# Performance work log

Measured on AMD Instinct MI355X. Metric: run time of the kernel, lower is better.

The kernel has to match this reference:

```python
import jax, jax.numpy as jnp
from jax import lax
import numpy as np

NEG = -1e30  # safe log-space -inf for fp32 (avoids inf-inf NaNs)
EPS = 1e-7   # keras.backend.epsilon()


def setup_inputs() -> dict:
    key = jax.random.key(0)
    k1, k2 = jax.random.split(key)
    B, T, C, L = 512, 512, 96, 64
    y_true = jax.random.randint(k1, (B, L), 0, C - 1, dtype=jnp.int64)  # labels in [0, C-2]
    # y_pred mimics softmax output: positive, rows sum to 1
    logits = jax.random.uniform(k2, (B, T, C), dtype=jnp.float32)
    y_pred = logits / jnp.sum(logits, axis=-1, keepdims=True)
    return {"y_true": y_true, "y_pred": y_pred}


def _ctc_batch_cost(y_true, y_pred):
    # Faithful to keras.backend.ctc_batch_cost with full input/label lengths
    # and blank index = num_classes - 1.
    B, T, C = y_pred.shape
    L = y_true.shape[1]
    blank = C - 1
    S = 2 * L + 1  # extended label length: blanks interleaved

    logp = jnp.log(y_pred + EPS)  # [B, T, C]

    # extended label sequence: blank, l0, blank, l1, ..., blank
    ext = jnp.full((B, S), blank, dtype=y_true.dtype).at[:, 1::2].set(y_true)  # [B, S]

    # log-probs of extended labels at every time step: [T, B, S]
    lp = jnp.take_along_axis(
        logp, jnp.broadcast_to(ext[:, None, :], (B, T, S)), axis=2
    ).transpose(1, 0, 2)

    # skip transition (s-2 -> s) allowed iff ext[s] != blank and ext[s] != ext[s-2]
    skip = jnp.concatenate(
        [jnp.zeros((B, 2), dtype=bool),
         (ext[:, 2:] != blank) & (ext[:, 2:] != ext[:, :-2])],
        axis=1,
    )  # [B, S]

    # init: alpha_0(0) = logp(blank), alpha_0(1) = logp(l0)
    alpha0 = jnp.full((B, S), NEG, dtype=logp.dtype)
    alpha0 = alpha0.at[:, 0].set(lp[0, :, 0]).at[:, 1].set(lp[0, :, 1])

    def step(alpha, lp_t):
        s1 = jnp.pad(alpha[:, :-1], ((0, 0), (1, 0)), constant_values=NEG)
        s2 = jnp.pad(alpha[:, :-2], ((0, 0), (2, 0)), constant_values=NEG)
        a = jnp.logaddexp(alpha, s1)
        a = jnp.where(skip, jnp.logaddexp(a, s2), a)
        return a + lp_t, None

    alpha, _ = lax.scan(step, alpha0, lp[1:])
    loss = -jnp.logaddexp(alpha[:, -1], alpha[:, -2])  # [B]
    return loss[:, None]  # [B, 1], matching ctc_batch_cost


def reference(y_true, y_pred):
    return _ctc_batch_cost(y_true, y_pred)
```

## Files before the change

kernel.cpp:

```cpp
#include <hip/hip_runtime.h>
#include <math.h>


constexpr int Bv = 512;
constexpr int Tv = 512;
constexpr int Cv = 96;
constexpr int Lv = 64;
constexpr int BLANK = Cv - 1;
constexpr float EPSf = 1e-7f;

constexpr int ROWS = 32;
constexpr int NCH  = Tv / ROWS;
constexpr int CF   = ROWS * Cv;
constexpr int RS   = 100;
constexpr int LBUF = ROWS * RS;

__device__ __forceinline__ float dpp_shr1(float x) {
    return __int_as_float(
        __builtin_amdgcn_update_dpp(0, __float_as_int(x), 0x138, 0xf, 0xf, true));
}
template <int C>
__device__ __forceinline__ float dppmax(float m) {
    return fmaxf(m, __int_as_float(
        __builtin_amdgcn_update_dpp(0, __float_as_int(m), C, 0xf, 0xf, true)));
}

__global__ void __launch_bounds__(64, 1) ctc_fwd(const int* __restrict__ y_true,
                                                 const float* __restrict__ y_pred,
                                                 float* __restrict__ out) {
    __shared__ float lds[2 * LBUF];

    const int b = blockIdx.x;
    const int l = threadIdx.x;
    const float* __restrict__ yp = y_pred + (size_t)b * (Tv * Cv);

    const int lab   = y_true[b * Lv + l];
    const int labm1 = __shfl_up(lab, 1);
    const bool skip = (l > 0) && (lab != labm1);

#define WA(i) ((((i)*64 + l) / 24) * 400 + (((i)*64 + l) % 24) * 16)
    const int wa0 = WA(0),  wa1 = WA(1),  wa2 = WA(2),  wa3 = WA(3);
    const int wa4 = WA(4),  wa5 = WA(5),  wa6 = WA(6),  wa7 = WA(7);
    const int wa8 = WA(8),  wa9 = WA(9), wa10 = WA(10), wa11 = WA(11);
#undef WA

    float4 G0, G1, G2, G3, G4, G5, G6, G7, G8, G9, G10, G11;
    float4 H0, H1, H2, H3, H4, H5, H6, H7, H8, H9, H10, H11;
#define GLOADS(S, g) do { const float* gp_ = (g) + l * 4;                    \
    S##0 = *(const float4*)(gp_ +    0); S##1 = *(const float4*)(gp_ +  256);\
    S##2 = *(const float4*)(gp_ +  512); S##3 = *(const float4*)(gp_ +  768);\
    S##4 = *(const float4*)(gp_ + 1024); S##5 = *(const float4*)(gp_ + 1280);\
    S##6 = *(const float4*)(gp_ + 1536); S##7 = *(const float4*)(gp_ + 1792);\
    S##8 = *(const float4*)(gp_ + 2048); S##9 = *(const float4*)(gp_ + 2304);\
    S##10= *(const float4*)(gp_ + 2560); S##11= *(const float4*)(gp_ + 2816);} while (0)
#define E4(v) make_float4((v).x + EPSf, (v).y + EPSf, (v).z + EPSf, (v).w + EPSf)
#define SWRITES(S, bufn) do { char* p_ = (char*)(bufn);                      \
    *(float4*)(p_ + wa0) = E4(S##0);  *(float4*)(p_ + wa1) = E4(S##1);       \
    *(float4*)(p_ + wa2) = E4(S##2);  *(float4*)(p_ + wa3) = E4(S##3);       \
    *(float4*)(p_ + wa4) = E4(S##4);  *(float4*)(p_ + wa5) = E4(S##5);       \
    *(float4*)(p_ + wa6) = E4(S##6);  *(float4*)(p_ + wa7) = E4(S##7);       \
    *(float4*)(p_ + wa8) = E4(S##8);  *(float4*)(p_ + wa9) = E4(S##9);       \
    *(float4*)(p_ + wa10)= E4(S##10); *(float4*)(p_ + wa11)= E4(S##11); } while (0)

    float AB0,AB1,AB2,AB3,AB4,AB5,AB6,AB7, AL0,AL1,AL2,AL3,AL4,AL5,AL6,AL7;
    float BB0,BB1,BB2,BB3,BB4,BB5,BB6,BB7, BL0,BL1,BL2,BL3,BL4,BL5,BL6,BL7;
#define LOAD8(P, bb, r0) do { const float* pB_ = (bb) + BLANK;               \
    const float* pL_ = (bb) + lab;                                           \
    P##B0 = pB_[((r0)+0)*RS]; P##L0 = pL_[((r0)+0)*RS];                      \
    P##B1 = pB_[((r0)+1)*RS]; P##L1 = pL_[((r0)+1)*RS];                      \
    P##B2 = pB_[((r0)+2)*RS]; P##L2 = pL_[((r0)+2)*RS];                      \
    P##B3 = pB_[((r0)+3)*RS]; P##L3 = pL_[((r0)+3)*RS];                      \
    P##B4 = pB_[((r0)+4)*RS]; P##L4 = pL_[((r0)+4)*RS];                      \
    P##B5 = pB_[((r0)+5)*RS]; P##L5 = pL_[((r0)+5)*RS];                      \
    P##B6 = pB_[((r0)+6)*RS]; P##L6 = pL_[((r0)+6)*RS];                      \
    P##B7 = pB_[((r0)+7)*RS]; P##L7 = pL_[((r0)+7)*RS]; } while (0)

    float a0, a1, a2;
    int   e_acc = 0;
    float sc_p = 1.0f; int e_p = 0;

    auto step = [&](float pb, float pl) {
        float pls = skip ? pl : 0.0f;
        float a1p = dpp_shr1(a1);
        float t01 = a0 + a1;
        float na1 = fmaf(a1p, pls, t01 * pl);
        float na0 = fmaf(a1p, pb, a0 * pb);
        float na2 = (a2 + a1) * pb;
        a0 = na0; a1 = na1; a2 = na2;
    };
    auto rn_apply = [&]() {
        a0 *= sc_p; a1 *= sc_p; a2 *= sc_p; e_acc += e_p;
    };
    auto rn_compute = [&]() {
        float m = fmaxf(fmaxf(a0, a1), a2);
        m = dppmax<0x111>(m); m = dppmax<0x112>(m); m = dppmax<0x114>(m);
        m = dppmax<0x118>(m); m = dppmax<0x142>(m); m = dppmax<0x143>(m);
        float mw = __int_as_float(__builtin_amdgcn_readlane(__float_as_int(m), 63));
        int e; (void)frexpf(mw, &e);
        sc_p = ldexpf(1.0f, -e); e_p = e;
    };
#define GROUP8(P) do {                                                       \
    step(P##B0, P##L0); step(P##B1, P##L1); step(P##B2, P##L2);              \
    step(P##B3, P##L3); rn_apply();                                          \
    step(P##B4, P##L4); step(P##B5, P##L5); step(P##B6, P##L6);              \
    step(P##B7, P##L7); rn_compute(); } while (0)

    GLOADS(G, yp);
    GLOADS(H, yp + CF);
    SWRITES(G, lds);
    GLOADS(G, yp + 2 * CF);
    LOAD8(A, lds, 0);
    const bool lane0 = (l == 0);
    a0 = lane0 ? AB0 : 0.0f;
    a1 = lane0 ? AL0 : 0.0f;
    a2 = 0.0f;

    float* const buf0 = lds;
    float* const buf1 = lds + LBUF;

    for (int c = 0; c < NCH; c += 2) {
        LOAD8(B, buf0, 8);
        if (c == 0) {
            step(AB1, AL1); step(AB2, AL2); step(AB3, AL3); rn_apply();
            step(AB4, AL4); step(AB5, AL5); step(AB6, AL6); step(AB7, AL7);
            rn_compute();
        } else {
            GROUP8(A);
        }
        LOAD8(A, buf0, 16);
        GROUP8(B);
        LOAD8(B, buf0, 24);
        GROUP8(A);
        SWRITES(H, buf1);
        if (c + 3 < NCH) GLOADS(H, yp + (size_t)(c + 3) * CF);
        LOAD8(A, buf1, 0);
        GROUP8(B);

        LOAD8(B, buf1, 8);
        GROUP8(A);
        LOAD8(A, buf1, 16);
        GROUP8(B);
        LOAD8(B, buf1, 24);
        GROUP8(A);
        if (c + 1 < NCH - 1) SWRITES(G, buf0);
        if (c + 4 < NCH) GLOADS(G, yp + (size_t)(c + 4) * CF);
        if (c + 1 < NCH - 1) LOAD8(A, buf0, 0);
        GROUP8(B);
    }

    if (l == 63) {
        float sum = a1 + a2;
        out[b] = -(logf(sum) + (float)e_acc * 0.69314718055994530942f);
    }
#undef GLOADS
#undef SWRITES
#undef E4
#undef LOAD8
#undef GROUP8
}

extern "C" void kernel_launch(void* const* d_in, const int* in_sizes, int n_in,
                              void* d_out, int out_size, void* d_ws, size_t ws_size,
                              hipStream_t stream) {
    const int*   y_true = (const int*)d_in[0];
    const float* y_pred = (const float*)d_in[1];
    float*       out    = (float*)d_out;
    (void)in_sizes; (void)n_in; (void)out_size; (void)d_ws; (void)ws_size;
    ctc_fwd<<<Bv, 64, 0, stream>>>(y_true, y_pred, out);
}
```

Measured before the change: 149.8 us.

## Split producer and consumer into separate wavefronts with double-buffered LDS

The block grows to two wavefronts. One wave only streams y_pred chunks from global memory into the LDS double buffer, and the other runs the CTC alpha recursion from LDS, with __syncthreads between halves. The goal is to take global-load issue and LDS writes off the latency-critical recursion wave so the two overlap on separate waves. In exchange, each half-chunk now costs a block barrier, and the grid uses more waves per CU.

```diff
diff --git a/kernel.cpp b/kernel.cpp
--- a/kernel.cpp
+++ b/kernel.cpp
@@ -25,13 +25,15 @@
         __builtin_amdgcn_update_dpp(0, __float_as_int(m), C, 0xf, 0xf, true)));
 }
 
-__global__ void __launch_bounds__(64, 1) ctc_fwd(const int* __restrict__ y_true,
-                                                 const float* __restrict__ y_pred,
-                                                 float* __restrict__ out) {
+__global__ void __launch_bounds__(128, 1) ctc_fwd(const int* __restrict__ y_true,
+                                                  const float* __restrict__ y_pred,
+                                                  float* __restrict__ out) {
     __shared__ float lds[2 * LBUF];
 
-    const int b = blockIdx.x;
-    const int l = threadIdx.x;
+    const int b   = blockIdx.x;
+    const int tid = threadIdx.x;
+    const int wid = tid >> 6;
+    const int l   = tid & 63;
     const float* __restrict__ yp = y_pred + (size_t)b * (Tv * Cv);
 
     const int lab   = y_true[b * Lv + l];
@@ -78,6 +80,7 @@
     float a0, a1, a2;
     int   e_acc = 0;
     float sc_p = 1.0f; int e_p = 0;
+    const bool lane0 = (l == 0);
 
     auto step = [&](float pb, float pl) {
         float pls = skip ? pl : 0.0f;
@@ -105,50 +108,55 @@
     step(P##B4, P##L4); step(P##B5, P##L5); step(P##B6, P##L6);              \
     step(P##B7, P##L7); rn_compute(); } while (0)
 
-    GLOADS(G, yp);
-    GLOADS(H, yp + CF);
-    SWRITES(G, lds);
-    GLOADS(G, yp + 2 * CF);
-    LOAD8(A, lds, 0);
-    const bool lane0 = (l == 0);
-    a0 = lane0 ? AB0 : 0.0f;
-    a1 = lane0 ? AL0 : 0.0f;
-    a2 = 0.0f;
+#define CONSUME(bb, FIRST) do {                                              \
+    LOAD8(A, (bb), 0);                                                       \
+    LOAD8(B, (bb), 8);                                                       \
+    if (FIRST) {                                                             \
+        a0 = lane0 ? AB0 : 0.0f;          \
+        a1 = lane0 ? AL0 : 0.0f;                                             \
+        a2 = 0.0f;                                                           \
+        step(AB1, AL1); step(AB2, AL2); step(AB3, AL3); rn_apply();          \
+        step(AB4, AL4); step(AB5, AL5); step(AB6, AL6); step(AB7, AL7);      \
+        rn_compute();                                                        \
+    } else {                                                                 \
+        GROUP8(A);                                                           \
+    }                                                                        \
+    LOAD8(A, (bb), 16);                                                      \
+    GROUP8(B);                                                               \
+    LOAD8(B, (bb), 24);                                                      \
+    GROUP8(A);                                                               \
+    GROUP8(B);                                                               \
+} while (0)
 
     float* const buf0 = lds;
     float* const buf1 = lds + LBUF;
 
+    if (wid) {
+        GLOADS(G, yp);
+        GLOADS(H, yp + CF);
+        SWRITES(G, lds);
+        GLOADS(G, yp + 2 * CF);
+    }
+    __syncthreads();
+
     for (int c = 0; c < NCH; c += 2) {
-        LOAD8(B, buf0, 8);
-        if (c == 0) {
-            step(AB1, AL1); step(AB2, AL2); step(AB3, AL3); rn_apply();
-            step(AB4, AL4); step(AB5, AL5); step(AB6, AL6); step(AB7, AL7);
-            rn_compute();
+        if (wid) {
+            SWRITES(H, buf1);
+            if (c + 3 < NCH) GLOADS(H, yp + (size_t)(c + 3) * CF);
         } else {
-            GROUP8(A);
+            CONSUME(buf0, c == 0);
         }
-        LOAD8(A, buf0, 16);
-        GROUP8(B);
-        LOAD8(B, buf0, 24);
-        GROUP8(A);
-        SWRITES(H, buf1);
-        if (c + 3 < NCH) GLOADS(H, yp + (size_t)(c + 3) * CF);
-        LOAD8(A, buf1, 0);
-        GROUP8(B);
-
-        LOAD8(B, buf1, 8);
-        GROUP8(A);
-        LOAD8(A, buf1, 16);
-        GROUP8(B);
-        LOAD8(B, buf1, 24);
-        GROUP8(A);
-        if (c + 1 < NCH - 1) SWRITES(G, buf0);
-        if (c + 4 < NCH) GLOADS(G, yp + (size_t)(c + 4) * CF);
-        if (c + 1 < NCH - 1) LOAD8(A, buf0, 0);
-        GROUP8(B);
+        __syncthreads();
+        if (wid) {
+            if (c + 2 < NCH) SWRITES(G, buf0);
+            if (c + 4 < NCH) GLOADS(G, yp + (size_t)(c + 4) * CF);
+        } else {
+            CONSUME(buf1, false);
+        }
+        __syncthreads();
     }
 
-    if (l == 63) {
+    if (tid == 63) {
         float sum = a1 + a2;
         out[b] = -(logf(sum) + (float)e_acc * 0.69314718055994530942f);
     }
@@ -157,6 +165,7 @@
 #undef E4
 #undef LOAD8
 #undef GROUP8
+#undef CONSUME
 }
 
 extern "C" void kernel_launch(void* const* d_in, const int* in_sizes, int n_in,
@@ -166,5 +175,5 @@
     const float* y_pred = (const float*)d_in[1];
     float*       out    = (float*)d_out;
     (void)in_sizes; (void)n_in; (void)out_size; (void)d_ws; (void)ws_size;
-    ctc_fwd<<<Bv, 64, 0, stream>>>(y_true, y_pred, out);
+    ctc_fwd<<<Bv, 128, 0, stream>>>(y_true, y_pred, out);
 }
```

Result: no change. 149.8 us (-0.0%).
